# Performance work log

Measured on AMD Instinct MI355X. Metric: run time of the kernel, lower is better.

Reference implementation:

```python
import jax, jax.numpy as jnp
import numpy as np

B = 4096
IN = 1024      # input_shape * 2
H = 2048       # rnn_hidden_dim * 2
A = 64         # n_actions
A2 = A * A     # fc2 output width


def setup_inputs() -> dict:
    key = jax.random.key(0)
    ks = jax.random.split(key, 12)
    s_in = 1.0 / np.sqrt(IN)
    s_h = 1.0 / np.sqrt(H)
    return {
        "inputs": jax.random.normal(ks[0], (B, IN), jnp.float32),
        "hidden_state": jax.random.normal(ks[1], (B, H), jnp.float32),
        # fc1: Linear(IN -> H)
        "W1": jax.random.uniform(ks[2], (H, IN), jnp.float32, -s_in, s_in),
        "b1": jax.random.uniform(ks[3], (H,), jnp.float32, -s_in, s_in),
        # GRUCell(H -> H), gate order r, z, n
        "Wih": jax.random.uniform(ks[4], (3 * H, H), jnp.float32, -s_h, s_h),
        "Whh": jax.random.uniform(ks[5], (3 * H, H), jnp.float32, -s_h, s_h),
        "bih": jax.random.uniform(ks[6], (3 * H,), jnp.float32, -s_h, s_h),
        "bhh": jax.random.uniform(ks[7], (3 * H,), jnp.float32, -s_h, s_h),
        # fc2: Linear(H -> A^2)
        "W2": jax.random.uniform(ks[8], (A2, H), jnp.float32, -s_h, s_h),
        "b2": jax.random.uniform(ks[9], (A2,), jnp.float32, -s_h, s_h),
    }


# Static gather indices for the vectorized __decode_combined_output.
# Row 2i, col j: max over q[i, j : j+A]  (contiguous window)
_IDX1 = np.arange(A)[:, None] + np.arange(A)[None, :]              # [A, A]
# Row 2i+1, col j: max over q[i, k-1] for k in range(j, A^2, A);
# at j=0 the index k-1 = -1 wraps to the last element (torch semantics).
_IDX2 = (np.arange(A)[:, None] + np.arange(A)[None, :] * A - 1) % A2  # [A, A]


def reference(inputs, hidden_state, W1, b1, Wih, Whh, bih, bhh, W2, b2):
    x = jax.nn.relu(inputs @ W1.T + b1)                 # [B, H]
    h_in = hidden_state.reshape(-1, H)
    gi = x @ Wih.T + bih                                # [B, 3H]
    gh = h_in @ Whh.T + bhh                             # [B, 3H]
    ir, iz, inn = jnp.split(gi, 3, axis=1)
    hr, hz, hn = jnp.split(gh, 3, axis=1)
    r = jax.nn.sigmoid(ir + hr)
    z = jax.nn.sigmoid(iz + hz)
    n = jnp.tanh(inn + r * hn)
    h = (1.0 - z) * n + z * h_in                        # [B, H]
    q = h @ W2.T + b2                                   # [B, A^2]
    q1 = jnp.max(q[:, _IDX1], axis=-1)                  # [B, A]
    q2 = jnp.max(q[:, _IDX2], axis=-1)                  # [B, A]
    out = jnp.stack([q1, q2], axis=1).reshape(-1, A)    # interleaved [2B, A]
    return out, h
```

## Files before the change

### kernel.cpp

```cpp
#include <hip/hip_runtime.h>
#include <stdint.h>

typedef unsigned short u16;
typedef __bf16 bf16x8 __attribute__((ext_vector_type(8)));
typedef float f32x4 __attribute__((ext_vector_type(4)));
typedef u16 u16x8 __attribute__((ext_vector_type(8)));

__device__ __forceinline__ float b2f(u16 v) {
    union { float f; unsigned int u; } x; x.u = ((unsigned int)v) << 16; return x.f;
}
__device__ __forceinline__ u16 f2b(float f) {
    union { float f; unsigned int u; } x; x.f = f;
    unsigned int r = x.u + 0x7fff + ((x.u >> 16) & 1);
    return (u16)(r >> 16);
}

__device__ __forceinline__ void gll16(const void* g, void* l) {
    __builtin_amdgcn_global_load_lds(
        (const __attribute__((address_space(1))) void*)g,
        (__attribute__((address_space(3))) void*)l,
        16, 0, 0);
}

__device__ __forceinline__ bf16x8 pack8(float4 f0, float4 f1) {
    union { float4 f; uint4 u; } a, b;
    a.f = f0; b.f = f1;
    const unsigned sel = 0x07060302u;
    union { unsigned u[4]; bf16x8 v; } r;
    r.u[0] = __builtin_amdgcn_perm(a.u.y + 0x8000u, a.u.x + 0x8000u, sel);
    r.u[1] = __builtin_amdgcn_perm(a.u.w + 0x8000u, a.u.z + 0x8000u, sel);
    r.u[2] = __builtin_amdgcn_perm(b.u.y + 0x8000u, b.u.x + 0x8000u, sel);
    r.u[3] = __builtin_amdgcn_perm(b.u.w + 0x8000u, b.u.z + 0x8000u, sel);
    return r.v;
}

__global__ __launch_bounds__(256) void cvt_kernel(
    const float* __restrict__ s, u16* __restrict__ d)
{
    const size_t i = ((size_t)blockIdx.x * 256 + threadIdx.x) * 8;
    float4 f0 = *(const float4*)(s + i);
    float4 f1 = *(const float4*)(s + i + 4);
    union { bf16x8 v; u16x8 u; } r;
    r.v = pack8(f0, f1);
    *(u16x8*)(d + i) = r.u;
}

template <bool RELU>
__global__ __launch_bounds__(256, 4) void gemm_bt(
    const u16* __restrict__ A, const u16* __restrict__ Bw,
    const float* __restrict__ bias, u16* __restrict__ C,
    int M, int N, int K)
{
    __shared__ alignas(16) u16 sA[128 * 64];
    __shared__ alignas(16) u16 sB[128 * 64];

    const int t = threadIdx.x;
    const int l = t & 63;
    const int w = t >> 6;
    const int mBase = blockIdx.y * 128;
    const int nBase = blockIdx.x * 128;
    const int wr = w >> 1, wc = w & 1;

    f32x4 acc[4][4] = {};

    const int frow = l & 15;
    const int cIdx = l >> 4;

    for (int k0 = 0; k0 < K; k0 += 64) {
#pragma unroll
        for (int i = 0; i < 4; ++i) {
            const int phys = i * 256 + t;
            const int r = phys >> 3;
            const int c = (phys & 7) ^ (r & 7);
            gll16(A + (size_t)(mBase + r) * K + (k0 + c * 8),
                  (char*)sA + (i * 256 + w * 64) * 16);
            gll16(Bw + (size_t)(nBase + r) * K + (k0 + c * 8),
                  (char*)sB + (i * 256 + w * 64) * 16);
        }

        __syncthreads();

#pragma unroll
        for (int s = 0; s < 2; ++s) {
            bf16x8 af[4], bf[4];
#pragma unroll
            for (int rr = 0; rr < 4; ++rr) {
                const int fr = wr * 64 + rr * 16 + frow;
                af[rr] = *(const bf16x8*)((char*)sA +
                         (fr * 8 + ((s * 4 + cIdx) ^ (fr & 7))) * 16);
            }
#pragma unroll
            for (int cc = 0; cc < 4; ++cc) {
                const int fr = wc * 64 + cc * 16 + frow;
                bf[cc] = *(const bf16x8*)((char*)sB +
                         (fr * 8 + ((s * 4 + cIdx) ^ (fr & 7))) * 16);
            }
#pragma unroll
            for (int r = 0; r < 4; ++r)
#pragma unroll
                for (int c = 0; c < 4; ++c)
                    acc[r][c] = __builtin_amdgcn_mfma_f32_16x16x32_bf16(
                        af[r], bf[c], acc[r][c], 0, 0, 0);
        }

        __syncthreads();
    }

    const int rquad = (l >> 4) * 4;
#pragma unroll
    for (int c = 0; c < 4; ++c) {
        const int col = nBase + wc * 64 + c * 16 + (l & 15);
        const float bv = bias[col];
#pragma unroll
        for (int r = 0; r < 4; ++r) {
            const int row = mBase + wr * 64 + r * 16 + rquad;
#pragma unroll
            for (int i = 0; i < 4; ++i) {
                float v = acc[r][c][i] + bv;
                if (RELU) v = fmaxf(v, 0.0f);
                C[(size_t)(row + i) * N + col] = f2b(v);
            }
        }
    }
}

__global__ __launch_bounds__(256) void gru_kernel(
    const u16* __restrict__ gi, const u16* __restrict__ gh,
    const float* __restrict__ hprev, float* __restrict__ houtf,
    u16* __restrict__ houtb, int H)
{
    const size_t idx = ((size_t)blockIdx.x * 256 + threadIdx.x) * 8;
    const size_t b = idx / H;
    const size_t j = idx - b * H;
    const size_t g0 = b * (size_t)(3 * H) + j;

    u16x8 vir = *(const u16x8*)&gi[g0];
    u16x8 viz = *(const u16x8*)&gi[g0 + H];
    u16x8 vin = *(const u16x8*)&gi[g0 + 2 * H];
    u16x8 vhr = *(const u16x8*)&gh[g0];
    u16x8 vhz = *(const u16x8*)&gh[g0 + H];
    u16x8 vhn = *(const u16x8*)&gh[g0 + 2 * H];
    float4 hp0 = *(const float4*)&hprev[idx];
    float4 hp1 = *(const float4*)&hprev[idx + 4];
    float hp[8] = {hp0.x, hp0.y, hp0.z, hp0.w, hp1.x, hp1.y, hp1.z, hp1.w};
    float ho[8];
    u16x8 ob;
#pragma unroll
    for (int i = 0; i < 8; ++i) {
        float r = 1.f / (1.f + expf(-(b2f(vir[i]) + b2f(vhr[i]))));
        float z = 1.f / (1.f + expf(-(b2f(viz[i]) + b2f(vhz[i]))));
        float n = tanhf(b2f(vin[i]) + r * b2f(vhn[i]));
        float h = (1.f - z) * n + z * hp[i];
        ho[i] = h;
        ob[i] = f2b(h);
    }
    *(float4*)&houtf[idx]     = make_float4(ho[0], ho[1], ho[2], ho[3]);
    *(float4*)&houtf[idx + 4] = make_float4(ho[4], ho[5], ho[6], ho[7]);
    *(u16x8*)&houtb[idx] = ob;
}

__global__ __launch_bounds__(256) void decode_kernel(
    const u16* __restrict__ q, float* __restrict__ out)
{
    __shared__ float s[4096];
    const int row = blockIdx.x;
    const int t = threadIdx.x;
    const size_t base = (size_t)row * 4096;
#pragma unroll
    for (int i = 0; i < 16; ++i) {
        int j = t + i * 256;
        s[j] = b2f(q[base + j]);
    }
    __syncthreads();
    if (t < 64) {
        float m = -INFINITY;
#pragma unroll 8
        for (int k = 0; k < 64; ++k) m = fmaxf(m, s[t + k]);
        out[(size_t)(2 * row) * 64 + t] = m;
    } else if (t < 128) {
        const int rr = t - 64;
        float m = -INFINITY;
#pragma unroll 8
        for (int k = 0; k < 64; ++k) m = fmaxf(m, s[rr + 64 * k]);
        const int j = (rr + 1) & 63;
        out[(size_t)(2 * row + 1) * 64 + j] = m;
    }
}

extern "C" void kernel_launch(void* const* d_in, const int* in_sizes, int n_in,
                              void* d_out, int out_size, void* d_ws, size_t ws_size,
                              hipStream_t stream) {
    constexpr int Bn = 4096, IN = 1024, H = 2048, A = 64, A2 = A * A;
    constexpr size_t BH  = (size_t)Bn * H;
    constexpr size_t H3H = (size_t)3 * H * H;
    constexpr size_t HIN = (size_t)H * IN;
    constexpr size_t BIN = (size_t)Bn * IN;
    constexpr size_t A2H = (size_t)A2 * H;
    constexpr size_t B3H = (size_t)Bn * 3 * H;
    constexpr size_t BA2 = (size_t)Bn * A2;

    const float* inputs = (const float*)d_in[0];
    const float* h0     = (const float*)d_in[1];
    const float* W1     = (const float*)d_in[2];
    const float* b1     = (const float*)d_in[3];
    const float* Wih    = (const float*)d_in[4];
    const float* Whh    = (const float*)d_in[5];
    const float* bih    = (const float*)d_in[6];
    const float* bhh    = (const float*)d_in[7];
    const float* W2     = (const float*)d_in[8];
    const float* b2     = (const float*)d_in[9];

    float* out  = (float*)d_out;
    float* hout = out + (size_t)2 * Bn * A;

    u16* wsu  = (u16*)d_ws;
    u16* h0b  = wsu;
    u16* Whhb = wsu + BH;
    u16* Wihb = wsu;
    u16* W1b  = wsu + H3H;
    u16* inb  = wsu + H3H + HIN;
    u16* x    = wsu + BH + H3H;
    u16* gi   = x + BH;
    u16* gh   = gi + B3H;
    u16* hbf  = gh + B3H;
    u16* q    = gi;
    u16* W2b  = gi + BA2;

    dim3 blk(256);
    cvt_kernel<<<dim3(BH  / 2048), blk, 0, stream>>>(h0,  h0b);
    cvt_kernel<<<dim3(H3H / 2048), blk, 0, stream>>>(Whh, Whhb);
    gemm_bt<false><<<dim3(3 * H / 128, Bn / 128), blk, 0, stream>>>(
        h0b, Whhb, bhh, gh, Bn, 3 * H, H);
    cvt_kernel<<<dim3(HIN / 2048), blk, 0, stream>>>(W1, W1b);
    cvt_kernel<<<dim3(BIN / 2048), blk, 0, stream>>>(inputs, inb);
    cvt_kernel<<<dim3(H3H / 2048), blk, 0, stream>>>(Wih, Wihb);
    gemm_bt<true><<<dim3(H / 128, Bn / 128), blk, 0, stream>>>(
        inb, W1b, b1, x, Bn, H, IN);
    gemm_bt<false><<<dim3(3 * H / 128, Bn / 128), blk, 0, stream>>>(
        x, Wihb, bih, gi, Bn, 3 * H, H);
    gru_kernel<<<dim3((Bn * H / 8) / 256), blk, 0, stream>>>(
        gi, gh, h0, hout, hbf, H);
    cvt_kernel<<<dim3(A2H / 2048), blk, 0, stream>>>(W2, W2b);
    gemm_bt<false><<<dim3(A2 / 128, Bn / 128), blk, 0, stream>>>(
        hbf, W2b, b2, q, Bn, A2, H);
    decode_kernel<<<dim3(Bn), blk, 0, stream>>>(q, out);
}
```

Baseline: 538.2 us.

## Replace GEMM with 256x256 double-buffered pipelined kernel and XCD-aware remapping

```diff
diff --git a/kernel.cpp b/kernel.cpp
--- a/kernel.cpp
+++ b/kernel.cpp
@@ -45,80 +45,192 @@
     *(u16x8*)(d + i) = r.u;
 }
 
+
+#define FBAR() do { asm volatile("" ::: "memory"); \
+                    __builtin_amdgcn_s_barrier();  \
+                    asm volatile("" ::: "memory"); } while (0)
+#define WAIT_LGKM0() asm volatile("s_waitcnt lgkmcnt(0)" ::: "memory")
+#define WAIT_VM6()   asm volatile("s_waitcnt vmcnt(6)" ::: "memory")
+#define WAIT_VM0()   asm volatile("s_waitcnt vmcnt(0)" ::: "memory")
+
+__device__ __forceinline__ void stage_half(
+    const u16* __restrict__ Mp, int rowBase, int K, int k0,
+    u16* region, int t, int w)
+{
+#pragma unroll
+    for (int it = 0; it < 2; ++it) {
+        const int phys = it * 512 + t;
+        const int r = phys >> 3;
+        const int c = (phys & 7) ^ (r & 7);
+        gll16(Mp + (size_t)(rowBase + r) * K + (k0 + c * 8),
+              (char*)region + (it * 512 + w * 64) * 16);
+    }
+}
+
+__device__ __forceinline__ void ld_a(const u16* region, int ra, int g0,
+                                     bf16x8 (&out)[4][2])
+{
+#pragma unroll
+    for (int mi = 0; mi < 4; ++mi)
+#pragma unroll
+        for (int s = 0; s < 2; ++s) {
+            const int lr = mi * 32 + ra;
+            out[mi][s] = *(const bf16x8*)((const char*)region +
+                         (lr * 8 + ((s * 4 + g0) ^ (lr & 7))) * 16);
+        }
+}
+
+__device__ __forceinline__ void ld_b(const u16* region, int rb, int g0,
+                                     bf16x8 (&out)[2][2])
+{
+#pragma unroll
+    for (int ni = 0; ni < 2; ++ni)
+#pragma unroll
+        for (int s = 0; s < 2; ++s) {
+            const int lr = ni * 64 + rb;
+            out[ni][s] = *(const bf16x8*)((const char*)region +
+                         (lr * 8 + ((s * 4 + g0) ^ (lr & 7))) * 16);
+        }
+}
+
+template <int MO, int NO>
+__device__ __forceinline__ void mfma_quad(const bf16x8 (&af)[4][2],
+                                          const bf16x8 (&bf)[2][2],
+                                          f32x4 (&acc)[8][4])
+{
+    __builtin_amdgcn_s_setprio(1);
+#pragma unroll
+    for (int mi = 0; mi < 4; ++mi)
+#pragma unroll
+        for (int ni = 0; ni < 2; ++ni)
+#pragma unroll
+            for (int s = 0; s < 2; ++s)
+                acc[MO + mi][NO + ni] = __builtin_amdgcn_mfma_f32_16x16x32_bf16(
+                    af[mi][s], bf[ni][s], acc[MO + mi][NO + ni], 0, 0, 0);
+    __builtin_amdgcn_s_setprio(0);
+}
+
 template <bool RELU>
-__global__ __launch_bounds__(256, 4) void gemm_bt(
+__global__ __launch_bounds__(512, 2) void gemm256(
     const u16* __restrict__ A, const u16* __restrict__ Bw,
     const float* __restrict__ bias, u16* __restrict__ C,
     int M, int N, int K)
 {
-    __shared__ alignas(16) u16 sA[128 * 64];
-    __shared__ alignas(16) u16 sB[128 * 64];
+    (void)M;
+    __shared__ alignas(16) u16 L[2][4][8192];
 
     const int t = threadIdx.x;
     const int l = t & 63;
     const int w = t >> 6;
-    const int mBase = blockIdx.y * 128;
-    const int nBase = blockIdx.x * 128;
-    const int wr = w >> 1, wc = w & 1;
-
-    f32x4 acc[4][4] = {};
+    const int wr = w >> 2;
+    const int wc = w & 3;
+
+    const int gx = gridDim.x;
+    const int nwg = gx * gridDim.y;
+    const int orig = blockIdx.y * gx + blockIdx.x;
+    const int q8 = nwg >> 3, r8 = nwg & 7;
+    const int xcd = orig & 7, rem = orig >> 3;
+    const int wg = (xcd < r8 ? xcd * (q8 + 1)
+                             : r8 * (q8 + 1) + (xcd - r8) * q8) + rem;
+    const int mBase = (wg / gx) * 256;
+    const int nBase = (wg % gx) * 256;
 
     const int frow = l & 15;
-    const int cIdx = l >> 4;
-
-    for (int k0 = 0; k0 < K; k0 += 64) {
-#pragma unroll
-        for (int i = 0; i < 4; ++i) {
-            const int phys = i * 256 + t;
-            const int r = phys >> 3;
-            const int c = (phys & 7) ^ (r & 7);
-            gll16(A + (size_t)(mBase + r) * K + (k0 + c * 8),
-                  (char*)sA + (i * 256 + w * 64) * 16);
-            gll16(Bw + (size_t)(nBase + r) * K + (k0 + c * 8),
-                  (char*)sB + (i * 256 + w * 64) * 16);
-        }
-
-        __syncthreads();
-
-#pragma unroll
-        for (int s = 0; s < 2; ++s) {
-            bf16x8 af[4], bf[4];
-#pragma unroll
-            for (int rr = 0; rr < 4; ++rr) {
-                const int fr = wr * 64 + rr * 16 + frow;
-                af[rr] = *(const bf16x8*)((char*)sA +
-                         (fr * 8 + ((s * 4 + cIdx) ^ (fr & 7))) * 16);
-            }
-#pragma unroll
-            for (int cc = 0; cc < 4; ++cc) {
-                const int fr = wc * 64 + cc * 16 + frow;
-                bf[cc] = *(const bf16x8*)((char*)sB +
-                         (fr * 8 + ((s * 4 + cIdx) ^ (fr & 7))) * 16);
-            }
-#pragma unroll
-            for (int r = 0; r < 4; ++r)
-#pragma unroll
-                for (int c = 0; c < 4; ++c)
-                    acc[r][c] = __builtin_amdgcn_mfma_f32_16x16x32_bf16(
-                        af[r], bf[c], acc[r][c], 0, 0, 0);
-        }
-
-        __syncthreads();
-    }
-
-    const int rquad = (l >> 4) * 4;
-#pragma unroll
-    for (int c = 0; c < 4; ++c) {
-        const int col = nBase + wc * 64 + c * 16 + (l & 15);
+    const int g0 = l >> 4;
+    const int ra = wr * 16 + frow;
+    const int rb = wc * 16 + frow;
+
+    f32x4 acc[8][4] = {};
+    bf16x8 a0[4][2], a1[4][2], b0[2][2], b1[2][2];
+
+    const int NI = K >> 7;
+
+    stage_half(A,  mBase,       K, 0,  &L[0][0][0], t, w);
+    stage_half(Bw, nBase,       K, 0,  &L[0][2][0], t, w);
+    stage_half(Bw, nBase + 128, K, 0,  &L[0][3][0], t, w);
+    stage_half(A,  mBase + 128, K, 0,  &L[0][1][0], t, w);
+    stage_half(A,  mBase,       K, 64, &L[1][0][0], t, w);
+    stage_half(Bw, nBase,       K, 64, &L[1][2][0], t, w);
+    stage_half(Bw, nBase + 128, K, 64, &L[1][3][0], t, w);
+    WAIT_VM6();
+    FBAR();
+
+    for (int i = 0; i < NI; ++i) {
+        const bool nl = (i + 1 < NI);
+        const int kT1 = (2 * i + 1) << 6;
+        const int kT2 = (2 * i + 2) << 6;
+        const int kT3 = (2 * i + 3) << 6;
+
+        ld_a(&L[0][0][0], ra, g0, a0);
+        ld_b(&L[0][2][0], rb, g0, b0);
+        stage_half(A, mBase + 128, K, kT1, &L[1][1][0], t, w);
+        FBAR();
+        WAIT_LGKM0();
+        mfma_quad<0, 0>(a0, b0, acc);
+        FBAR();
+
+        ld_b(&L[0][3][0], rb, g0, b1);
+        if (nl) stage_half(A, mBase, K, kT2, &L[0][0][0], t, w);
+        FBAR();
+        WAIT_LGKM0();
+        mfma_quad<0, 2>(a0, b1, acc);
+        FBAR();
+
+        ld_a(&L[0][1][0], ra, g0, a1);
+        if (nl) stage_half(Bw, nBase, K, kT2, &L[0][2][0], t, w);
+        FBAR();
+        WAIT_LGKM0();
+        mfma_quad<4, 0>(a1, b0, acc);
+        FBAR();
+
+        if (nl) stage_half(Bw, nBase + 128, K, kT2, &L[0][3][0], t, w);
+        FBAR();
+        mfma_quad<4, 2>(a1, b1, acc);
+        if (nl) { WAIT_VM6(); } else { WAIT_VM0(); }
+        FBAR();
+
+        ld_a(&L[1][0][0], ra, g0, a0);
+        ld_b(&L[1][2][0], rb, g0, b0);
+        if (nl) stage_half(A, mBase + 128, K, kT2, &L[0][1][0], t, w);
+        FBAR();
+        WAIT_LGKM0();
+        mfma_quad<0, 0>(a0, b0, acc);
+        FBAR();
+
+        ld_b(&L[1][3][0], rb, g0, b1);
+        if (nl) stage_half(A, mBase, K, kT3, &L[1][0][0], t, w);
+        FBAR();
+        WAIT_LGKM0();
+        mfma_quad<0, 2>(a0, b1, acc);
+        FBAR();
+
+        ld_a(&L[1][1][0], ra, g0, a1);
+        if (nl) stage_half(Bw, nBase, K, kT3, &L[1][2][0], t, w);
+        FBAR();
+        WAIT_LGKM0();
+        mfma_quad<4, 0>(a1, b0, acc);
+        FBAR();
+
+        if (nl) stage_half(Bw, nBase + 128, K, kT3, &L[1][3][0], t, w);
+        FBAR();
+        mfma_quad<4, 2>(a1, b1, acc);
+        if (nl) { WAIT_VM6(); }
+        FBAR();
+    }
+
+    const int rq = (l >> 4) * 4;
+#pragma unroll
+    for (int ni = 0; ni < 4; ++ni) {
+        const int col = nBase + ni * 64 + wc * 16 + (l & 15);
         const float bv = bias[col];
 #pragma unroll
-        for (int r = 0; r < 4; ++r) {
-            const int row = mBase + wr * 64 + r * 16 + rquad;
-#pragma unroll
-            for (int i = 0; i < 4; ++i) {
-                float v = acc[r][c][i] + bv;
+        for (int mi = 0; mi < 8; ++mi) {
+            const int row = mBase + mi * 32 + wr * 16 + rq;
+#pragma unroll
+            for (int i2 = 0; i2 < 4; ++i2) {
+                float v = acc[mi][ni][i2] + bv;
                 if (RELU) v = fmaxf(v, 0.0f);
-                C[(size_t)(row + i) * N + col] = f2b(v);
+                C[(size_t)(row + i2) * N + col] = f2b(v);
             }
         }
     }
@@ -227,21 +339,22 @@
     u16* W2b  = gi + BA2;
 
     dim3 blk(256);
+    dim3 gblk(512);
     cvt_kernel<<<dim3(BH  / 2048), blk, 0, stream>>>(h0,  h0b);
     cvt_kernel<<<dim3(H3H / 2048), blk, 0, stream>>>(Whh, Whhb);
-    gemm_bt<false><<<dim3(3 * H / 128, Bn / 128), blk, 0, stream>>>(
+    gemm256<false><<<dim3(3 * H / 256, Bn / 256), gblk, 0, stream>>>(
         h0b, Whhb, bhh, gh, Bn, 3 * H, H);
     cvt_kernel<<<dim3(HIN / 2048), blk, 0, stream>>>(W1, W1b);
     cvt_kernel<<<dim3(BIN / 2048), blk, 0, stream>>>(inputs, inb);
     cvt_kernel<<<dim3(H3H / 2048), blk, 0, stream>>>(Wih, Wihb);
-    gemm_bt<true><<<dim3(H / 128, Bn / 128), blk, 0, stream>>>(
+    gemm256<true><<<dim3(H / 256, Bn / 256), gblk, 0, stream>>>(
         inb, W1b, b1, x, Bn, H, IN);
-    gemm_bt<false><<<dim3(3 * H / 128, Bn / 128), blk, 0, stream>>>(
+    gemm256<false><<<dim3(3 * H / 256, Bn / 256), gblk, 0, stream>>>(
         x, Wihb, bih, gi, Bn, 3 * H, H);
     gru_kernel<<<dim3((Bn * H / 8) / 256), blk, 0, stream>>>(
         gi, gh, h0, hout, hbf, H);
     cvt_kernel<<<dim3(A2H / 2048), blk, 0, stream>>>(W2, W2b);
-    gemm_bt<false><<<dim3(A2 / 128, Bn / 128), blk, 0, stream>>>(
+    gemm256<false><<<dim3(A2 / 256, Bn / 256), gblk, 0, stream>>>(
         hbf, W2b, b2, q, Bn, A2, H);
     decode_kernel<<<dim3(Bn), blk, 0, stream>>>(q, out);
 }
```

Measured after the change: 576.1 us. +7.1%, slower.
